# Performance work log

Hardware: AMD Instinct MI355X
Metric: run time of the kernel (lower is better)

Reference implementation:

```python
import jax, jax.numpy as jnp
import numpy as np

GAMMA = 0.1
N_CENTERS = 1024
INPUT_DIM = 64
BATCH = 65536


def setup_inputs() -> dict:
    key = jax.random.key(0)
    kx, kc = jax.random.split(key)
    x = jax.random.normal(kx, (BATCH, INPUT_DIM), dtype=jnp.float32)
    # centers ~ Uniform(0, 1), matching torch.empty(...).uniform_(0, 1)
    centers = jax.random.uniform(kc, (N_CENTERS, INPUT_DIM), dtype=jnp.float32)
    return {"x": x, "centers": centers}


def reference(x, centers):
    # Pairwise squared L2 distance via the matmul expansion trick:
    x_sq = jnp.sum(x * x, axis=-1, keepdims=True)          # [B, 1]
    c_sq = jnp.sum(centers * centers, axis=-1)             # [N]
    cross = jnp.einsum("bd,nd->bn", x, centers)            # [B, N]
    l2 = x_sq + c_sq[None, :] - 2.0 * cross                # [B, N]
    l2 = jnp.maximum(l2, 0.0)  # guard tiny negatives from the expansion
    return jnp.exp(-GAMMA * l2)
```

## Files before the change

### kernel.cpp

```cpp
#include <hip/hip_runtime.h>

#define GAMMA 0.1f

constexpr int MTOT = 65536;
constexpr int NTOT = 1024;
constexpr int KDIM = 64;
constexpr int BM = 64;
constexpr int BN = 128;
constexpr int NTIL = 16;

using frag_ab = __attribute__((ext_vector_type(8))) short;
using f32x4   = __attribute__((ext_vector_type(4))) float;

typedef __attribute__((address_space(1))) const unsigned int gu32;
typedef __attribute__((address_space(3))) unsigned int lu32;

__device__ __forceinline__ ushort bf16_rne(float x, float& back) {
  unsigned u = __float_as_uint(x);
  unsigned r = (u + 0x7FFFu + ((u >> 16) & 1u)) >> 16;
  back = __uint_as_float(r << 16);
  return (ushort)r;
}

__global__ __launch_bounds__(512, 4)
void rbf_persistent_kernel(const float* __restrict__ x,
                           const float* __restrict__ centers,
                           float* __restrict__ out) {
  __shared__ ushort sChi[BN * KDIM];
  __shared__ ushort sClo[BN * KDIM];
  __shared__ float  sCsq[BN];
  __shared__ __align__(16) float sX[2][BM * KDIM];

  const int tid = threadIdx.x;
  const int nt = blockIdx.x & 7;
  const int mg = blockIdx.x >> 3;

  auto issue_x = [&](int mt, int b) {
    const char* src = reinterpret_cast<const char*>(x) + (size_t)mt * BM * KDIM * 4;
    char* dst = reinterpret_cast<char*>(&sX[b][0]);
    #pragma unroll
    for (int p = 0; p < 2; ++p) {
      const int q = p * 512 + tid;
      const int row = q >> 4;
      const int s = q & 15;
      const int sc = (row << 4) | (s ^ (row & 15));
      __builtin_amdgcn_global_load_lds((gu32*)(src + (size_t)sc * 16),
                                       (lu32*)(dst + (size_t)q * 16), 16, 0, 0);
    }
  };

  issue_x(mg, 0);

  #pragma unroll
  for (int pass = 0; pass < 2; ++pass) {
    const int idx = pass * 4096 + tid * 8;
    const int row = idx >> 6;
    const int s = tid & 7;
    const float4* p = reinterpret_cast<const float4*>(
        centers + (size_t)nt * BN * KDIM + idx);
    float4 v0 = p[0], v1 = p[1];
    float v[8] = {v0.x, v0.y, v0.z, v0.w, v1.x, v1.y, v1.z, v1.w};
    frag_ab hv, lv;
    float ss = 0.0f;
    #pragma unroll
    for (int i = 0; i < 8; ++i) {
      float back;
      ushort hb = bf16_rne(v[i], back);
      float b2;
      ushort lb = bf16_rne(v[i] - back, b2);
      (void)b2;
      ss += v[i] * v[i];
      hv[i] = (short)hb;
      lv[i] = (short)lb;
    }
    ss += __shfl_xor(ss, 1);
    ss += __shfl_xor(ss, 2);
    ss += __shfl_xor(ss, 4);
    if (s == 0) sCsq[row] = ss;
    const int slot = s ^ (row & 7);
    *reinterpret_cast<frag_ab*>(sChi + row * 64 + slot * 8) = hv;
    *reinterpret_cast<frag_ab*>(sClo + row * 64 + slot * 8) = lv;
  }
  __syncthreads();

  const int lane = tid & 63;
  const int wave = tid >> 6;
  const int wm = wave & 3;
  const int wn = wave >> 2;
  const int l = lane & 15;
  const int g = lane >> 4;

  frag_ab ch[4][2];
  #pragma unroll
  for (int nf = 0; nf < 4; ++nf) {
    #pragma unroll
    for (int ks = 0; ks < 2; ++ks) {
      const int row = wn * 64 + nf * 16 + l;
      const int slot = (ks * 4 + g) ^ (l & 7);
      ch[nf][ks] = *reinterpret_cast<const frag_ab*>(sChi + row * 64 + slot * 8);
    }
  }
  float4 csq4[4];
  #pragma unroll
  for (int nf = 0; nf < 4; ++nf)
    csq4[nf] = *reinterpret_cast<const float4*>(&sCsq[wn * 64 + nf * 16 + g * 4]);

  const int ncol0 = nt * BN + wn * 64;

  #pragma unroll 1
  for (int j = 0; j < NTIL; ++j) {
    const int mt = mg + 64 * j;
    const int b = j & 1;

    float ss = 0.0f;
    frag_ab xh[2], xl[2];
    #pragma unroll
    for (int ks = 0; ks < 2; ++ks) {
      const int cb = ks * 8 + g * 2;
      const float* base = &sX[b][(wm * 16 + l) * KDIM];
      const float4 a0 = *reinterpret_cast<const float4*>(base + ((cb) ^ l) * 4);
      const float4 a1 = *reinterpret_cast<const float4*>(base + ((cb + 1) ^ l) * 4);
      float v[8] = {a0.x, a0.y, a0.z, a0.w, a1.x, a1.y, a1.z, a1.w};
      frag_ab h, lo_;
      #pragma unroll
      for (int i = 0; i < 8; ++i) {
        float back;
        ushort hb = bf16_rne(v[i], back);
        float b2;
        ushort lb = bf16_rne(v[i] - back, b2);
        (void)b2;
        ss += v[i] * v[i];
        h[i] = (short)hb;
        lo_[i] = (short)lb;
      }
      xh[ks] = h;
      xl[ks] = lo_;
    }
    ss += __shfl_xor(ss, 16);
    ss += __shfl_xor(ss, 32);

    if (j + 1 < NTIL) issue_x(mg + 64 * (j + 1), b ^ 1);

    f32x4 acc[4] = {};
    #pragma unroll
    for (int ks = 0; ks < 2; ++ks) {
      #pragma unroll
      for (int nf = 0; nf < 4; ++nf) {
        const int row = wn * 64 + nf * 16 + l;
        const int slot = (ks * 4 + g) ^ (l & 7);
        const frag_ab cl = *reinterpret_cast<const frag_ab*>(sClo + row * 64 + slot * 8);
        acc[nf] = __builtin_amdgcn_mfma_f32_16x16x32_bf16(ch[nf][ks], xh[ks], acc[nf], 0, 0, 0);
        acc[nf] = __builtin_amdgcn_mfma_f32_16x16x32_bf16(ch[nf][ks], xl[ks], acc[nf], 0, 0, 0);
        acc[nf] = __builtin_amdgcn_mfma_f32_16x16x32_bf16(cl, xh[ks], acc[nf], 0, 0, 0);
      }
    }

    const size_t rowg = (size_t)mt * BM + wm * 16 + l;
    float* orow = out + rowg * (size_t)NTOT + ncol0;
    #pragma unroll
    for (int nf = 0; nf < 4; ++nf) {
      const f32x4 a = acc[nf];
      const float4 cs = csq4[nf];
      float4 o;
      o.x = __expf(-GAMMA * fmaxf(ss + cs.x - 2.0f * a[0], 0.0f));
      o.y = __expf(-GAMMA * fmaxf(ss + cs.y - 2.0f * a[1], 0.0f));
      o.z = __expf(-GAMMA * fmaxf(ss + cs.z - 2.0f * a[2], 0.0f));
      o.w = __expf(-GAMMA * fmaxf(ss + cs.w - 2.0f * a[3], 0.0f));
      *reinterpret_cast<float4*>(orow + nf * 16 + g * 4) = o;
    }

    __syncthreads();
  }
}

extern "C" void kernel_launch(void* const* d_in, const int* in_sizes, int n_in,
                              void* d_out, int out_size, void* d_ws, size_t ws_size,
                              hipStream_t stream) {
  (void)in_sizes; (void)n_in; (void)d_ws; (void)ws_size; (void)out_size;
  const float* x       = (const float*)d_in[0];
  const float* centers = (const float*)d_in[1];
  float* out = (float*)d_out;
  rbf_persistent_kernel<<<512, 512, 0, stream>>>(x, centers, out);
}
```

Measured before the change: 69.04 us.

## Precompute center bf16 splits in a prepass and stream centers per x-tile

Adds a small prepass kernel that converts the centers once to hi/lo bf16 halves plus squared norms in the workspace. The main kernel is restructured so each block keeps one 64-row x tile resident (converted once) and loops over all 1024 centers in 64-column chunks, double-buffered into LDS with global_load_lds. This removes the per-tile x conversion repeated across the 8 N-tile blocks and the redundant center conversion in all 512 blocks. In exchange it adds a second kernel launch, launches 1024 non-persistent blocks, and reads csq from global memory in the epilogue.

```diff
diff --git a/kernel.cpp b/kernel.cpp
--- a/kernel.cpp
+++ b/kernel.cpp
@@ -5,9 +5,9 @@
 constexpr int MTOT = 65536;
 constexpr int NTOT = 1024;
 constexpr int KDIM = 64;
-constexpr int BM = 64;
-constexpr int BN = 128;
-constexpr int NTIL = 16;
+constexpr int BM   = 64;
+constexpr int BNT  = 64;
+constexpr int NIT  = NTOT / BNT;
 
 using frag_ab = __attribute__((ext_vector_type(8))) short;
 using f32x4   = __attribute__((ext_vector_type(4))) float;
@@ -15,49 +15,81 @@
 typedef __attribute__((address_space(1))) const unsigned int gu32;
 typedef __attribute__((address_space(3))) unsigned int lu32;
 
-__device__ __forceinline__ ushort bf16_rne(float x, float& back) {
-  unsigned u = __float_as_uint(x);
+constexpr size_t WS_CHI = 0;
+constexpr size_t WS_CLO = 131072;
+constexpr size_t WS_CSQ = 262144;
+constexpr size_t WS_NEEDED = 262144 + 4096;
+
+__device__ __forceinline__ ushort bf16_rne(float v, float& back) {
+  unsigned u = __float_as_uint(v);
   unsigned r = (u + 0x7FFFu + ((u >> 16) & 1u)) >> 16;
   back = __uint_as_float(r << 16);
   return (ushort)r;
 }
 
+__global__ __launch_bounds__(256)
+void cen_convert_kernel(const float* __restrict__ centers,
+                        ushort* __restrict__ hi, ushort* __restrict__ lo,
+                        float* __restrict__ sq) {
+  const int c = blockIdx.x * 256 + threadIdx.x;
+  const int row = c >> 3;
+  const int s = c & 7;
+  const float4* p = reinterpret_cast<const float4*>(centers + (size_t)row * KDIM + s * 8);
+  float4 v0 = p[0], v1 = p[1];
+  float v[8] = {v0.x, v0.y, v0.z, v0.w, v1.x, v1.y, v1.z, v1.w};
+  frag_ab hv, lv;
+  float ss = 0.0f;
+  #pragma unroll
+  for (int i = 0; i < 8; ++i) {
+    float back;
+    ushort hb = bf16_rne(v[i], back);
+    float b2;
+    ushort lb = bf16_rne(v[i] - back, b2);
+    (void)b2;
+    ss += v[i] * v[i];
+    hv[i] = (short)hb;
+    lv[i] = (short)lb;
+  }
+  ss += __shfl_xor(ss, 1);
+  ss += __shfl_xor(ss, 2);
+  ss += __shfl_xor(ss, 4);
+  if (s == 0) sq[row] = ss;
+  const int slot = s ^ (row & 7);
+  *reinterpret_cast<frag_ab*>(hi + (size_t)row * KDIM + slot * 8) = hv;
+  *reinterpret_cast<frag_ab*>(lo + (size_t)row * KDIM + slot * 8) = lv;
+}
+
 __global__ __launch_bounds__(512, 4)
-void rbf_persistent_kernel(const float* __restrict__ x,
-                           const float* __restrict__ centers,
-                           float* __restrict__ out) {
-  __shared__ ushort sChi[BN * KDIM];
-  __shared__ ushort sClo[BN * KDIM];
-  __shared__ float  sCsq[BN];
-  __shared__ __align__(16) float sX[2][BM * KDIM];
+void rbf_main_kernel(const float* __restrict__ x,
+                     const ushort* __restrict__ chi,
+                     const ushort* __restrict__ clo,
+                     const float* __restrict__ csq,
+                     float* __restrict__ out) {
+  __shared__ ushort sXhi[BM * KDIM];
+  __shared__ ushort sXlo[BM * KDIM];
+  __shared__ float  sXsq[BM];
+  __shared__ ushort sCen[2][2 * BNT * KDIM];
 
   const int tid = threadIdx.x;
-  const int nt = blockIdx.x & 7;
-  const int mg = blockIdx.x >> 3;
+  const int mb  = blockIdx.x;
 
-  auto issue_x = [&](int mt, int b) {
-    const char* src = reinterpret_cast<const char*>(x) + (size_t)mt * BM * KDIM * 4;
-    char* dst = reinterpret_cast<char*>(&sX[b][0]);
-    #pragma unroll
-    for (int p = 0; p < 2; ++p) {
-      const int q = p * 512 + tid;
-      const int row = q >> 4;
-      const int s = q & 15;
-      const int sc = (row << 4) | (s ^ (row & 15));
-      __builtin_amdgcn_global_load_lds((gu32*)(src + (size_t)sc * 16),
-                                       (lu32*)(dst + (size_t)q * 16), 16, 0, 0);
-    }
+  auto issue_cen = [&](int nt, int b) {
+    const char* sH = reinterpret_cast<const char*>(chi) + (size_t)nt * BNT * KDIM * 2;
+    const char* sL = reinterpret_cast<const char*>(clo) + (size_t)nt * BNT * KDIM * 2;
+    char* d = reinterpret_cast<char*>(&sCen[b][0]);
+    __builtin_amdgcn_global_load_lds((gu32*)(sH + (size_t)tid * 16),
+                                     (lu32*)(d + (size_t)tid * 16), 16, 0, 0);
+    __builtin_amdgcn_global_load_lds((gu32*)(sL + (size_t)tid * 16),
+                                     (lu32*)(d + 8192 + (size_t)tid * 16), 16, 0, 0);
   };
 
-  issue_x(mg, 0);
+  issue_cen(0, 0);
 
-  #pragma unroll
-  for (int pass = 0; pass < 2; ++pass) {
-    const int idx = pass * 4096 + tid * 8;
-    const int row = idx >> 6;
-    const int s = tid & 7;
+  {
+    const int row = tid >> 3;
+    const int s   = tid & 7;
     const float4* p = reinterpret_cast<const float4*>(
-        centers + (size_t)nt * BN * KDIM + idx);
+        x + (size_t)mb * BM * KDIM + row * KDIM + s * 8);
     float4 v0 = p[0], v1 = p[1];
     float v[8] = {v0.x, v0.y, v0.z, v0.w, v1.x, v1.y, v1.z, v1.w};
     frag_ab hv, lv;
@@ -76,10 +108,10 @@
     ss += __shfl_xor(ss, 1);
     ss += __shfl_xor(ss, 2);
     ss += __shfl_xor(ss, 4);
-    if (s == 0) sCsq[row] = ss;
+    if (s == 0) sXsq[row] = ss;
     const int slot = s ^ (row & 7);
-    *reinterpret_cast<frag_ab*>(sChi + row * 64 + slot * 8) = hv;
-    *reinterpret_cast<frag_ab*>(sClo + row * 64 + slot * 8) = lv;
+    *reinterpret_cast<frag_ab*>(sXhi + row * 64 + slot * 8) = hv;
+    *reinterpret_cast<frag_ab*>(sXlo + row * 64 + slot * 8) = lv;
   }
   __syncthreads();
 
@@ -90,82 +122,52 @@
   const int l = lane & 15;
   const int g = lane >> 4;
 
-  frag_ab ch[4][2];
+  frag_ab xh[2], xl[2];
   #pragma unroll
-  for (int nf = 0; nf < 4; ++nf) {
+  for (int ks = 0; ks < 2; ++ks) {
+    const int row = wm * 16 + l;
+    const int slot = (ks * 4 + g) ^ (l & 7);
+    xh[ks] = *reinterpret_cast<const frag_ab*>(sXhi + row * 64 + slot * 8);
+    xl[ks] = *reinterpret_cast<const frag_ab*>(sXlo + row * 64 + slot * 8);
+  }
+  const float xs = sXsq[wm * 16 + l];
+
+  const size_t orow_base = ((size_t)mb * BM + wm * 16 + l) * (size_t)NTOT;
+
+  #pragma unroll 1
+  for (int nt = 0; nt < NIT; ++nt) {
+    const int b = nt & 1;
+    if (nt + 1 < NIT) issue_cen(nt + 1, b ^ 1);
+
+    const ushort* cH = &sCen[b][0];
+    const ushort* cL = &sCen[b][4096];
+
+    f32x4 acc[2] = {};
     #pragma unroll
     for (int ks = 0; ks < 2; ++ks) {
-      const int row = wn * 64 + nf * 16 + l;
       const int slot = (ks * 4 + g) ^ (l & 7);
-      ch[nf][ks] = *reinterpret_cast<const frag_ab*>(sChi + row * 64 + slot * 8);
-    }
-  }
-  float4 csq4[4];
-  #pragma unroll
-  for (int nf = 0; nf < 4; ++nf)
-    csq4[nf] = *reinterpret_cast<const float4*>(&sCsq[wn * 64 + nf * 16 + g * 4]);
-
-  const int ncol0 = nt * BN + wn * 64;
-
-  #pragma unroll 1
-  for (int j = 0; j < NTIL; ++j) {
-    const int mt = mg + 64 * j;
-    const int b = j & 1;
-
-    float ss = 0.0f;
-    frag_ab xh[2], xl[2];
-    #pragma unroll
-    for (int ks = 0; ks < 2; ++ks) {
-      const int cb = ks * 8 + g * 2;
-      const float* base = &sX[b][(wm * 16 + l) * KDIM];
-      const float4 a0 = *reinterpret_cast<const float4*>(base + ((cb) ^ l) * 4);
-      const float4 a1 = *reinterpret_cast<const float4*>(base + ((cb + 1) ^ l) * 4);
-      float v[8] = {a0.x, a0.y, a0.z, a0.w, a1.x, a1.y, a1.z, a1.w};
-      frag_ab h, lo_;
       #pragma unroll
-      for (int i = 0; i < 8; ++i) {
-        float back;
-        ushort hb = bf16_rne(v[i], back);
-        float b2;
-        ushort lb = bf16_rne(v[i] - back, b2);
-        (void)b2;
-        ss += v[i] * v[i];
-        h[i] = (short)hb;
-        lo_[i] = (short)lb;
-      }
-      xh[ks] = h;
-      xl[ks] = lo_;
-    }
-    ss += __shfl_xor(ss, 16);
-    ss += __shfl_xor(ss, 32);
-
-    if (j + 1 < NTIL) issue_x(mg + 64 * (j + 1), b ^ 1);
-
-    f32x4 acc[4] = {};
-    #pragma unroll
-    for (int ks = 0; ks < 2; ++ks) {
-      #pragma unroll
-      for (int nf = 0; nf < 4; ++nf) {
-        const int row = wn * 64 + nf * 16 + l;
-        const int slot = (ks * 4 + g) ^ (l & 7);
-        const frag_ab cl = *reinterpret_cast<const frag_ab*>(sClo + row * 64 + slot * 8);
-        acc[nf] = __builtin_amdgcn_mfma_f32_16x16x32_bf16(ch[nf][ks], xh[ks], acc[nf], 0, 0, 0);
-        acc[nf] = __builtin_amdgcn_mfma_f32_16x16x32_bf16(ch[nf][ks], xl[ks], acc[nf], 0, 0, 0);
+      for (int nf = 0; nf < 2; ++nf) {
+        const int row = wn * 32 + nf * 16 + l;
+        const frag_ab ch = *reinterpret_cast<const frag_ab*>(cH + row * 64 + slot * 8);
+        const frag_ab cl = *reinterpret_cast<const frag_ab*>(cL + row * 64 + slot * 8);
+        acc[nf] = __builtin_amdgcn_mfma_f32_16x16x32_bf16(ch, xh[ks], acc[nf], 0, 0, 0);
+        acc[nf] = __builtin_amdgcn_mfma_f32_16x16x32_bf16(ch, xl[ks], acc[nf], 0, 0, 0);
         acc[nf] = __builtin_amdgcn_mfma_f32_16x16x32_bf16(cl, xh[ks], acc[nf], 0, 0, 0);
       }
     }
 
-    const size_t rowg = (size_t)mt * BM + wm * 16 + l;
-    float* orow = out + rowg * (size_t)NTOT + ncol0;
+    const int ncol = nt * 64 + wn * 32;
+    float* orow = out + orow_base + ncol;
     #pragma unroll
-    for (int nf = 0; nf < 4; ++nf) {
+    for (int nf = 0; nf < 2; ++nf) {
+      const float4 cs = *reinterpret_cast<const float4*>(csq + ncol + nf * 16 + g * 4);
       const f32x4 a = acc[nf];
-      const float4 cs = csq4[nf];
       float4 o;
-      o.x = __expf(-GAMMA * fmaxf(ss + cs.x - 2.0f * a[0], 0.0f));
-      o.y = __expf(-GAMMA * fmaxf(ss + cs.y - 2.0f * a[1], 0.0f));
-      o.z = __expf(-GAMMA * fmaxf(ss + cs.z - 2.0f * a[2], 0.0f));
-      o.w = __expf(-GAMMA * fmaxf(ss + cs.w - 2.0f * a[3], 0.0f));
+      o.x = __expf(-GAMMA * fmaxf(xs + cs.x - 2.0f * a[0], 0.0f));
+      o.y = __expf(-GAMMA * fmaxf(xs + cs.y - 2.0f * a[1], 0.0f));
+      o.z = __expf(-GAMMA * fmaxf(xs + cs.z - 2.0f * a[2], 0.0f));
+      o.w = __expf(-GAMMA * fmaxf(xs + cs.w - 2.0f * a[3], 0.0f));
       *reinterpret_cast<float4*>(orow + nf * 16 + g * 4) = o;
     }
 
@@ -176,9 +178,16 @@
 extern "C" void kernel_launch(void* const* d_in, const int* in_sizes, int n_in,
                               void* d_out, int out_size, void* d_ws, size_t ws_size,
                               hipStream_t stream) {
-  (void)in_sizes; (void)n_in; (void)d_ws; (void)ws_size; (void)out_size;
+  (void)in_sizes; (void)n_in; (void)out_size; (void)ws_size;
   const float* x       = (const float*)d_in[0];
   const float* centers = (const float*)d_in[1];
   float* out = (float*)d_out;
-  rbf_persistent_kernel<<<512, 512, 0, stream>>>(x, centers, out);
+
+  char* ws = (char*)d_ws;
+  ushort* chi = (ushort*)(ws + WS_CHI);
+  ushort* clo = (ushort*)(ws + WS_CLO);
+  float*  csq = (float*)(ws + WS_CSQ);
+
+  cen_convert_kernel<<<32, 256, 0, stream>>>(centers, chi, clo, csq);
+  rbf_main_kernel<<<MTOT / BM, 512, 0, stream>>>(x, chi, clo, csq, out);
 }
```

New measurement: 73.74 us. 6.8% more time.

## Double row tile and precompute x bf16 split cooperatively in shared memory

Applied to the files above, without the earlier changes.

Raises the row tile per iteration from 64 to 128 so each wave computes two 16-row fragments and reuses each center fragment load across them. The x hi/lo bf16 split and row norms are now computed once per tile by all threads and stored in LDS, instead of being redone redundantly per wave. The async global-to-LDS copy becomes a register prefetch, and center hi fragments are read from LDS each tile instead of kept in registers. This adds a barrier per tile and more LDS traffic and register pressure.

```diff
diff --git a/kernel.cpp b/kernel.cpp
--- a/kernel.cpp
+++ b/kernel.cpp
@@ -5,51 +5,42 @@
 constexpr int MTOT = 65536;
 constexpr int NTOT = 1024;
 constexpr int KDIM = 64;
-constexpr int BM = 64;
+constexpr int BM = 128;
 constexpr int BN = 128;
-constexpr int NTIL = 16;
+constexpr int NTIL = 8;
 
 using frag_ab = __attribute__((ext_vector_type(8))) short;
+using bf16x4  = __attribute__((ext_vector_type(4))) short;
 using f32x4   = __attribute__((ext_vector_type(4))) float;
 
-typedef __attribute__((address_space(1))) const unsigned int gu32;
-typedef __attribute__((address_space(3))) unsigned int lu32;
-
-__device__ __forceinline__ ushort bf16_rne(float x, float& back) {
-  unsigned u = __float_as_uint(x);
+__device__ __forceinline__ ushort bf16_rne(float v, float& back) {
+  unsigned u = __float_as_uint(v);
   unsigned r = (u + 0x7FFFu + ((u >> 16) & 1u)) >> 16;
   back = __uint_as_float(r << 16);
   return (ushort)r;
 }
 
 __global__ __launch_bounds__(512, 4)
-void rbf_persistent_kernel(const float* __restrict__ x,
-                           const float* __restrict__ centers,
-                           float* __restrict__ out) {
+void rbf_kernel(const float* __restrict__ x,
+                const float* __restrict__ centers,
+                float* __restrict__ out) {
   __shared__ ushort sChi[BN * KDIM];
   __shared__ ushort sClo[BN * KDIM];
   __shared__ float  sCsq[BN];
-  __shared__ __align__(16) float sX[2][BM * KDIM];
+  __shared__ ushort sXhi[BM * KDIM];
+  __shared__ ushort sXlo[BM * KDIM];
+  __shared__ float  sXsq[BM];
 
   const int tid = threadIdx.x;
   const int nt = blockIdx.x & 7;
   const int mg = blockIdx.x >> 3;
 
-  auto issue_x = [&](int mt, int b) {
-    const char* src = reinterpret_cast<const char*>(x) + (size_t)mt * BM * KDIM * 4;
-    char* dst = reinterpret_cast<char*>(&sX[b][0]);
-    #pragma unroll
-    for (int p = 0; p < 2; ++p) {
-      const int q = p * 512 + tid;
-      const int row = q >> 4;
-      const int s = q & 15;
-      const int sc = (row << 4) | (s ^ (row & 15));
-      __builtin_amdgcn_global_load_lds((gu32*)(src + (size_t)sc * 16),
-                                       (lu32*)(dst + (size_t)q * 16), 16, 0, 0);
-    }
-  };
-
-  issue_x(mg, 0);
+  float4 rx[4];
+  {
+    const float4* p = reinterpret_cast<const float4*>(x + (size_t)mg * BM * KDIM);
+    #pragma unroll
+    for (int i = 0; i < 4; ++i) rx[i] = p[tid + 512 * i];
+  }
 
   #pragma unroll
   for (int pass = 0; pass < 2; ++pass) {
@@ -90,83 +81,111 @@
   const int l = lane & 15;
   const int g = lane >> 4;
 
-  frag_ab ch[4][2];
-  #pragma unroll
-  for (int nf = 0; nf < 4; ++nf) {
-    #pragma unroll
-    for (int ks = 0; ks < 2; ++ks) {
-      const int row = wn * 64 + nf * 16 + l;
-      const int slot = (ks * 4 + g) ^ (l & 7);
-      ch[nf][ks] = *reinterpret_cast<const frag_ab*>(sChi + row * 64 + slot * 8);
-    }
-  }
   float4 csq4[4];
   #pragma unroll
   for (int nf = 0; nf < 4; ++nf)
     csq4[nf] = *reinterpret_cast<const float4*>(&sCsq[wn * 64 + nf * 16 + g * 4]);
 
+  const int q16 = tid >> 4;
+  const int f15 = tid & 15;
   const int ncol0 = nt * BN + wn * 64;
 
   #pragma unroll 1
   for (int j = 0; j < NTIL; ++j) {
     const int mt = mg + 64 * j;
-    const int b = j & 1;
-
-    float ss = 0.0f;
-    frag_ab xh[2], xl[2];
+
+    float ssr[4];
+    #pragma unroll
+    for (int i = 0; i < 4; ++i) {
+      const int row = q16 + 32 * i;
+      const int s = f15 >> 1;
+      const int c = f15 & 1;
+      const float vv[4] = {rx[i].x, rx[i].y, rx[i].z, rx[i].w};
+      bf16x4 hv, lv;
+      float ss = 0.0f;
+      #pragma unroll
+      for (int e = 0; e < 4; ++e) {
+        float back;
+        ushort hb = bf16_rne(vv[e], back);
+        float b2;
+        ushort lb = bf16_rne(vv[e] - back, b2);
+        (void)b2;
+        ss += vv[e] * vv[e];
+        hv[e] = (short)hb;
+        lv[e] = (short)lb;
+      }
+      ssr[i] = ss;
+      const int slot = s ^ (row & 7);
+      *reinterpret_cast<bf16x4*>(sXhi + row * 64 + slot * 8 + c * 4) = hv;
+      *reinterpret_cast<bf16x4*>(sXlo + row * 64 + slot * 8 + c * 4) = lv;
+    }
+    #pragma unroll
+    for (int i = 0; i < 4; ++i) {
+      ssr[i] += __shfl_xor(ssr[i], 1);
+      ssr[i] += __shfl_xor(ssr[i], 2);
+      ssr[i] += __shfl_xor(ssr[i], 4);
+      ssr[i] += __shfl_xor(ssr[i], 8);
+    }
+    if (f15 == 0) {
+      #pragma unroll
+      for (int i = 0; i < 4; ++i) sXsq[q16 + 32 * i] = ssr[i];
+    }
+    __syncthreads();
+
+    if (j + 1 < NTIL) {
+      const float4* p = reinterpret_cast<const float4*>(
+          x + (size_t)(mg + 64 * (j + 1)) * BM * KDIM);
+      #pragma unroll
+      for (int i = 0; i < 4; ++i) rx[i] = p[tid + 512 * i];
+    }
+
+    frag_ab xh[2][2], xl[2][2];
+    float xs[2];
+    #pragma unroll
+    for (int mf = 0; mf < 2; ++mf) {
+      const int row = wm * 32 + mf * 16 + l;
+      xs[mf] = sXsq[row];
+      #pragma unroll
+      for (int ks = 0; ks < 2; ++ks) {
+        const int slot = (ks * 4 + g) ^ (l & 7);
+        xh[ks][mf] = *reinterpret_cast<const frag_ab*>(sXhi + row * 64 + slot * 8);
+        xl[ks][mf] = *reinterpret_cast<const frag_ab*>(sXlo + row * 64 + slot * 8);
+      }
+    }
+
+    f32x4 acc[4][2] = {};
     #pragma unroll
     for (int ks = 0; ks < 2; ++ks) {
-      const int cb = ks * 8 + g * 2;
-      const float* base = &sX[b][(wm * 16 + l) * KDIM];
-      const float4 a0 = *reinterpret_cast<const float4*>(base + ((cb) ^ l) * 4);
-      const float4 a1 = *reinterpret_cast<const float4*>(base + ((cb + 1) ^ l) * 4);
-      float v[8] = {a0.x, a0.y, a0.z, a0.w, a1.x, a1.y, a1.z, a1.w};
-      frag_ab h, lo_;
-      #pragma unroll
-      for (int i = 0; i < 8; ++i) {
-        float back;
-        ushort hb = bf16_rne(v[i], back);
-        float b2;
-        ushort lb = bf16_rne(v[i] - back, b2);
-        (void)b2;
-        ss += v[i] * v[i];
-        h[i] = (short)hb;
-        lo_[i] = (short)lb;
-      }
-      xh[ks] = h;
-      xl[ks] = lo_;
-    }
-    ss += __shfl_xor(ss, 16);
-    ss += __shfl_xor(ss, 32);
-
-    if (j + 1 < NTIL) issue_x(mg + 64 * (j + 1), b ^ 1);
-
-    f32x4 acc[4] = {};
-    #pragma unroll
-    for (int ks = 0; ks < 2; ++ks) {
+      const int slot = (ks * 4 + g) ^ (l & 7);
       #pragma unroll
       for (int nf = 0; nf < 4; ++nf) {
-        const int row = wn * 64 + nf * 16 + l;
-        const int slot = (ks * 4 + g) ^ (l & 7);
-        const frag_ab cl = *reinterpret_cast<const frag_ab*>(sClo + row * 64 + slot * 8);
-        acc[nf] = __builtin_amdgcn_mfma_f32_16x16x32_bf16(ch[nf][ks], xh[ks], acc[nf], 0, 0, 0);
-        acc[nf] = __builtin_amdgcn_mfma_f32_16x16x32_bf16(ch[nf][ks], xl[ks], acc[nf], 0, 0, 0);
-        acc[nf] = __builtin_amdgcn_mfma_f32_16x16x32_bf16(cl, xh[ks], acc[nf], 0, 0, 0);
-      }
-    }
-
-    const size_t rowg = (size_t)mt * BM + wm * 16 + l;
-    float* orow = out + rowg * (size_t)NTOT + ncol0;
-    #pragma unroll
-    for (int nf = 0; nf < 4; ++nf) {
-      const f32x4 a = acc[nf];
-      const float4 cs = csq4[nf];
-      float4 o;
-      o.x = __expf(-GAMMA * fmaxf(ss + cs.x - 2.0f * a[0], 0.0f));
-      o.y = __expf(-GAMMA * fmaxf(ss + cs.y - 2.0f * a[1], 0.0f));
-      o.z = __expf(-GAMMA * fmaxf(ss + cs.z - 2.0f * a[2], 0.0f));
-      o.w = __expf(-GAMMA * fmaxf(ss + cs.w - 2.0f * a[3], 0.0f));
-      *reinterpret_cast<float4*>(orow + nf * 16 + g * 4) = o;
+        const int crow = wn * 64 + nf * 16 + l;
+        const frag_ab ch = *reinterpret_cast<const frag_ab*>(sChi + crow * 64 + slot * 8);
+        const frag_ab cl = *reinterpret_cast<const frag_ab*>(sClo + crow * 64 + slot * 8);
+        #pragma unroll
+        for (int mf = 0; mf < 2; ++mf) {
+          acc[nf][mf] = __builtin_amdgcn_mfma_f32_16x16x32_bf16(ch, xh[ks][mf], acc[nf][mf], 0, 0, 0);
+          acc[nf][mf] = __builtin_amdgcn_mfma_f32_16x16x32_bf16(ch, xl[ks][mf], acc[nf][mf], 0, 0, 0);
+          acc[nf][mf] = __builtin_amdgcn_mfma_f32_16x16x32_bf16(cl, xh[ks][mf], acc[nf][mf], 0, 0, 0);
+        }
+      }
+    }
+
+    #pragma unroll
+    for (int mf = 0; mf < 2; ++mf) {
+      const size_t rowg = (size_t)mt * BM + wm * 32 + mf * 16 + l;
+      float* orow = out + rowg * (size_t)NTOT + ncol0;
+      #pragma unroll
+      for (int nf = 0; nf < 4; ++nf) {
+        const f32x4 a = acc[nf][mf];
+        const float4 cs = csq4[nf];
+        float4 o;
+        o.x = __expf(-GAMMA * fmaxf(xs[mf] + cs.x - 2.0f * a[0], 0.0f));
+        o.y = __expf(-GAMMA * fmaxf(xs[mf] + cs.y - 2.0f * a[1], 0.0f));
+        o.z = __expf(-GAMMA * fmaxf(xs[mf] + cs.z - 2.0f * a[2], 0.0f));
+        o.w = __expf(-GAMMA * fmaxf(xs[mf] + cs.w - 2.0f * a[3], 0.0f));
+        *reinterpret_cast<float4*>(orow + nf * 16 + g * 4) = o;
+      }
     }
 
     __syncthreads();
@@ -180,5 +199,5 @@
   const float* x       = (const float*)d_in[0];
   const float* centers = (const float*)d_in[1];
   float* out = (float*)d_out;
-  rbf_persistent_kernel<<<512, 512, 0, stream>>>(x, centers, out);
+  rbf_kernel<<<512, 512, 0, stream>>>(x, centers, out);
 }
```

Result: slower. 79.79 us (+15.6%).
